# Kernel tuning notes

Hardware: AMD Instinct MI355X
Metric: run time of the kernel (lower is better)

## Reference

```python
import jax, jax.numpy as jnp
import numpy as np

LN_EPS = 1e-5  # torch LayerNorm default

def _phi(x):
    # elu(x) + 1 feature map
    return jax.nn.elu(x) + 1.0

def setup_inputs() -> dict:
    key = jax.random.key(0)
    ks = jax.random.split(key, 5)
    B, N, D = 4, 8192, 1024
    s = 1.0 / np.sqrt(D)
    return {
        "H": jax.random.normal(ks[0], (B, N, D), dtype=jnp.float32),
        "W_qkv": jax.random.normal(ks[1], (3 * D, D), dtype=jnp.float32) * s,
        "b_qkv": jax.random.normal(ks[2], (3 * D,), dtype=jnp.float32) * 0.01,
        "W_proj": jax.random.normal(ks[3], (D, D), dtype=jnp.float32) * s,
        "b_proj": jax.random.normal(ks[4], (D,), dtype=jnp.float32) * 0.01,
        "gamma": jnp.ones((D,), dtype=jnp.float32),
        "beta": jnp.zeros((D,), dtype=jnp.float32),
    }

def reference(H, W_qkv, b_qkv, W_proj, b_proj, gamma, beta):
    B, N, D = H.shape
    num_heads = 16
    head_dim = D // num_heads
    residual = H
    # qkv projection: (B,N,3D)
    qkv = jnp.einsum('bnd,ed->bne', H, W_qkv) + b_qkv
    qkv = qkv.reshape(B, N, 3, num_heads, head_dim).transpose(2, 0, 3, 1, 4)
    q, k, v = qkv[0], qkv[1], qkv[2]  # each (B,h,N,d)
    q = _phi(q)
    k = _phi(k)
    # kv outer-product accumulated over nodes: (B,h,d,v)
    kv = jnp.einsum('bhnd,bhnv->bhdv', k, v)
    k1 = k.sum(axis=2)  # (B,h,d)
    qkv_out = jnp.einsum('bhnd,bhdv->bhnv', q, kv)
    qk1 = jnp.sum(q * k1[:, :, None, :], axis=-1, keepdims=True)
    out = qkv_out / jnp.clip(qk1, 1e-6, None)
    # NOTE: faithful to original -- reshape (B,h,N,d) -> (B,N,D) WITHOUT head transpose
    out = out.reshape(B, N, D)
    out = jnp.einsum('bnd,ed->bne', out, W_proj) + b_proj
    # LayerNorm over last dim
    mu = out.mean(axis=-1, keepdims=True)
    var = out.var(axis=-1, keepdims=True)
    out = (out - mu) * jax.lax.rsqrt(var + LN_EPS) * gamma + beta
    # dropout is identity at inference
    return out + residual
```

## Files before the change

### kernel.cpp

```cpp
#include <hip/hip_runtime.h>


typedef __attribute__((ext_vector_type(4))) float f32x4;
typedef __attribute__((ext_vector_type(8))) short bf16x8;

__device__ __forceinline__ unsigned short f2b(float f) {
    unsigned u = __float_as_uint(f);
    u = (u + 0x7FFFu + ((u >> 16) & 1u)) >> 16;
    return (unsigned short)u;
}
__device__ __forceinline__ float b2f(unsigned short h) {
    return __uint_as_float(((unsigned)h) << 16);
}

__device__ __forceinline__ void glds16(const void* gp, void* lp) {
    __builtin_amdgcn_global_load_lds(
        (__attribute__((address_space(1))) void*)(unsigned long long)gp,
        (__attribute__((address_space(3))) void*)(unsigned int)(unsigned long long)lp,
        16, 0, 0);
}

__global__ __launch_bounds__(256) void cvt_f32_bf16(const float* __restrict__ in,
                                                    unsigned short* __restrict__ out,
                                                    long n4) {
    long i = (long)blockIdx.x * 256 + threadIdx.x;
    long stride = (long)gridDim.x * 256;
    for (; i < n4; i += stride) {
        float4 v = ((const float4*)in)[i];
        ushort4 o;
        o.x = f2b(v.x); o.y = f2b(v.y); o.z = f2b(v.z); o.w = f2b(v.w);
        ((ushort4*)out)[i] = o;
    }
}

template<int MODE>
__global__ __launch_bounds__(512) void gemm256(const unsigned short* __restrict__ A,
                                               const unsigned short* __restrict__ B,
                                               const float* __restrict__ bias,
                                               void* __restrict__ Cout,
                                               int mb, int N, int K) {
    __shared__ unsigned short lds[2][2][256][64];
    const int tid = threadIdx.x;
    const int wid = tid >> 6, lane = tid & 63;
    const int wr = wid >> 2, wc = wid & 3;
    const int lr = lane & 15, lq = lane >> 4;
    const int cpx = (int)gridDim.x >> 3;
    const int L = ((int)blockIdx.x & 7) * cpx + ((int)blockIdx.x >> 3);
    const int bm = L % mb, bn = L / mb;
    const size_t aRow0 = (size_t)bm * 256, bRow0 = (size_t)bn * 256;

    const int sr8 = lane >> 3;
    const int ssw = ((lane & 7) ^ sr8) * 8;
    const unsigned short* aG = A + (aRow0 + (size_t)(wid * 8 + sr8)) * K + ssw;
    const unsigned short* bG = B + (bRow0 + (size_t)(wid * 8 + sr8)) * K + ssw;

    f32x4 acc[8][4] = {};
    const char* base = (const char*)&lds[0][0][0][0];

    auto stage = [&](int buf, int k0) {
#pragma unroll
        for (int j = 0; j < 8; ++j) {
            const unsigned short* g = (j < 4 ? aG : bG) + (size_t)(j & 3) * 64 * K + k0;
            glds16(g, &lds[buf][j >> 2][(j & 3) * 64 + wid * 8][0]);
        }
    };
    auto ldA = [&](int cur, int mi, int ks) {
        int row = wr * 128 + mi * 16 + lr;
        int off = (cur * 2 + 0) * 32768 + row * 128 + ((((ks << 2) | lq) ^ (row & 7)) << 4);
        return *(const bf16x8*)(base + off);
    };
    auto ldB = [&](int cur, int ni, int ks) {
        int row = wc * 64 + ni * 16 + lr;
        int off = (cur * 2 + 1) * 32768 + row * 128 + ((((ks << 2) | lq) ^ (row & 7)) << 4);
        return *(const bf16x8*)(base + off);
    };

    const int nt = K >> 6;
    stage(0, 0);
    asm volatile("s_waitcnt vmcnt(0)" ::: "memory");
    __builtin_amdgcn_s_barrier();

    bf16x8 af[4][2], bfr[4][2];
    for (int t = 0; t < nt; ++t) {
        const int cur = t & 1;
#pragma unroll
        for (int mi = 0; mi < 4; ++mi) {
            af[mi][0] = ldA(cur, mi, 0); af[mi][1] = ldA(cur, mi, 1);
        }
#pragma unroll
        for (int ni = 0; ni < 2; ++ni) {
            bfr[ni][0] = ldB(cur, ni, 0); bfr[ni][1] = ldB(cur, ni, 1);
        }
        if (t + 1 < nt) stage(cur ^ 1, (t + 1) << 6);
        __builtin_amdgcn_s_barrier();
        __builtin_amdgcn_s_setprio(1);
#pragma unroll
        for (int mi = 0; mi < 4; ++mi)
#pragma unroll
            for (int ni = 0; ni < 2; ++ni)
#pragma unroll
                for (int ks = 0; ks < 2; ++ks)
                    acc[mi][ni] = __builtin_amdgcn_mfma_f32_16x16x32_bf16(
                        af[mi][ks], bfr[ni][ks], acc[mi][ni], 0, 0, 0);
        __builtin_amdgcn_s_setprio(0);
        __builtin_amdgcn_s_barrier();
#pragma unroll
        for (int ni = 2; ni < 4; ++ni) {
            bfr[ni][0] = ldB(cur, ni, 0); bfr[ni][1] = ldB(cur, ni, 1);
        }
        __builtin_amdgcn_s_barrier();
        __builtin_amdgcn_s_setprio(1);
#pragma unroll
        for (int mi = 0; mi < 4; ++mi)
#pragma unroll
            for (int ni = 2; ni < 4; ++ni)
#pragma unroll
                for (int ks = 0; ks < 2; ++ks)
                    acc[mi][ni] = __builtin_amdgcn_mfma_f32_16x16x32_bf16(
                        af[mi][ks], bfr[ni][ks], acc[mi][ni], 0, 0, 0);
        __builtin_amdgcn_s_setprio(0);
        __builtin_amdgcn_s_barrier();
#pragma unroll
        for (int mi = 0; mi < 4; ++mi) {
            af[mi][0] = ldA(cur, mi + 4, 0); af[mi][1] = ldA(cur, mi + 4, 1);
        }
        __builtin_amdgcn_s_barrier();
        __builtin_amdgcn_s_setprio(1);
#pragma unroll
        for (int mi = 0; mi < 4; ++mi)
#pragma unroll
            for (int ni = 2; ni < 4; ++ni)
#pragma unroll
                for (int ks = 0; ks < 2; ++ks)
                    acc[mi + 4][ni] = __builtin_amdgcn_mfma_f32_16x16x32_bf16(
                        af[mi][ks], bfr[ni][ks], acc[mi + 4][ni], 0, 0, 0);
        __builtin_amdgcn_s_setprio(0);
        __builtin_amdgcn_s_barrier();
        __builtin_amdgcn_s_setprio(1);
#pragma unroll
        for (int mi = 0; mi < 4; ++mi)
#pragma unroll
            for (int ni = 0; ni < 2; ++ni)
#pragma unroll
                for (int ks = 0; ks < 2; ++ks)
                    acc[mi + 4][ni] = __builtin_amdgcn_mfma_f32_16x16x32_bf16(
                        af[mi][ks], bfr[ni][ks], acc[mi + 4][ni], 0, 0, 0);
        __builtin_amdgcn_s_setprio(0);
        asm volatile("s_waitcnt vmcnt(0)" ::: "memory");
        __builtin_amdgcn_s_barrier();
        __builtin_amdgcn_sched_barrier(0);
    }
#pragma unroll
    for (int mi = 0; mi < 8; ++mi) {
#pragma unroll
        for (int ni = 0; ni < 4; ++ni) {
            int col = (int)bRow0 + wc * 64 + ni * 16 + lr;
            float bv = bias[col];
#pragma unroll
            for (int r = 0; r < 4; ++r) {
                size_t row = aRow0 + wr * 128 + mi * 16 + lq * 4 + r;
                float v = acc[mi][ni][r] + bv;
                if (MODE == 0) {
                    if (col < 2048) v = (v > 0.f) ? (v + 1.f) : __expf(v);
                    ((unsigned short*)Cout)[row * (size_t)N + col] = f2b(v);
                } else {
                    ((float*)Cout)[row * (size_t)N + col] = v;
                }
            }
        }
    }
}

__global__ __launch_bounds__(256) void kv_partial(const unsigned short* __restrict__ qkv,
                                                  float* __restrict__ part) {
    const int bh = blockIdx.x, chunk = blockIdx.y;
    const int b = bh >> 4, h = bh & 15;
    __shared__ unsigned short kb[16][64];
    __shared__ unsigned short vb[16][64];
    const int tid = threadIdx.x;
    const int d0 = (tid >> 4) * 4, v0 = (tid & 15) * 4;
    float acc[4][4] = {};
    float k1a[4] = {0.f, 0.f, 0.f, 0.f};
    const size_t base = ((size_t)b * 8192 + (size_t)chunk * 1024) * 3072;
    const int nn = tid >> 4;
    const int which = (tid >> 3) & 1;
    const int cg = tid & 7;
    const size_t loff = base + (size_t)nn * 3072 + (which ? 2048 : 1024) + h * 64 + cg * 8;

    for (int n0 = 0; n0 < 1024; n0 += 16) {
        uint4 val = *(const uint4*)(qkv + loff + (size_t)n0 * 3072);
        if (which) *(uint4*)(&vb[nn][cg * 8]) = val;
        else       *(uint4*)(&kb[nn][cg * 8]) = val;
        __syncthreads();
#pragma unroll 4
        for (int j = 0; j < 16; ++j) {
            ushort4 ku = *(const ushort4*)(&kb[j][d0]);
            ushort4 vu = *(const ushort4*)(&vb[j][v0]);
            float kd[4] = {b2f(ku.x), b2f(ku.y), b2f(ku.z), b2f(ku.w)};
            float vd[4] = {b2f(vu.x), b2f(vu.y), b2f(vu.z), b2f(vu.w)};
#pragma unroll
            for (int i = 0; i < 4; ++i)
#pragma unroll
                for (int jj = 0; jj < 4; ++jj)
                    acc[i][jj] += kd[i] * vd[jj];
            if ((tid & 15) == 0)
#pragma unroll
                for (int i = 0; i < 4; ++i) k1a[i] += kd[i];
        }
        __syncthreads();
    }
    float* dst = part + ((size_t)bh * 8 + chunk) * 4160;
#pragma unroll
    for (int i = 0; i < 4; ++i)
#pragma unroll
        for (int jj = 0; jj < 4; ++jj)
            dst[(d0 + i) * 64 + v0 + jj] = acc[i][jj];
    if ((tid & 15) == 0)
#pragma unroll
        for (int i = 0; i < 4; ++i) dst[4096 + d0 + i] = k1a[i];
}

__global__ __launch_bounds__(256) void kv_reduce(const float* __restrict__ part,
                                                 float* __restrict__ kvk1) {
    const int bh = blockIdx.x;
    for (int idx = threadIdx.x; idx < 4160; idx += 256) {
        float s = 0.f;
#pragma unroll
        for (int c = 0; c < 8; ++c) s += part[((size_t)bh * 8 + c) * 4160 + idx];
        kvk1[(size_t)bh * 4160 + idx] = s;
    }
}

__global__ __launch_bounds__(256) void apply_attn(const unsigned short* __restrict__ qkv,
                                                  const float* __restrict__ kvk1,
                                                  unsigned short* __restrict__ att) {
    const int nblk = blockIdx.x;
    const int bh = blockIdx.y;
    const int b = bh >> 4, h = bh & 15;
    __shared__ float kvs[64][64];
    __shared__ float k1s[64];
    const float* src = kvk1 + (size_t)bh * 4160;
    for (int i = threadIdx.x; i < 4096; i += 256) kvs[i >> 6][i & 63] = src[i];
    if (threadIdx.x < 64) k1s[threadIdx.x] = src[4096 + threadIdx.x];
    __syncthreads();
    const int t = threadIdx.x;
    const int r = t >> 2, qt = t & 3;
    const int n = nblk * 64 + r;
    const unsigned short* qrow = qkv + ((size_t)b * 8192 + n) * 3072 + h * 64;
    float acc[16] = {};
    float qk1 = 0.f;
    for (int dc = 0; dc < 64; dc += 8) {
        uint4 qu = *(const uint4*)(qrow + dc);
        unsigned qw[4] = {qu.x, qu.y, qu.z, qu.w};
#pragma unroll
        for (int jj = 0; jj < 8; ++jj) {
            float qd = (jj & 1) ? __uint_as_float(qw[jj >> 1] & 0xFFFF0000u)
                                : __uint_as_float(qw[jj >> 1] << 16);
            int d = dc + jj;
            qk1 += qd * k1s[d];
            const float4* kr = (const float4*)(&kvs[d][qt * 16]);
            float4 c0 = kr[0], c1 = kr[1], c2 = kr[2], c3 = kr[3];
            acc[0]  += qd * c0.x; acc[1]  += qd * c0.y; acc[2]  += qd * c0.z; acc[3]  += qd * c0.w;
            acc[4]  += qd * c1.x; acc[5]  += qd * c1.y; acc[6]  += qd * c1.z; acc[7]  += qd * c1.w;
            acc[8]  += qd * c2.x; acc[9]  += qd * c2.y; acc[10] += qd * c2.z; acc[11] += qd * c2.w;
            acc[12] += qd * c3.x; acc[13] += qd * c3.y; acc[14] += qd * c3.z; acc[15] += qd * c3.w;
        }
    }
    float rinv = 1.f / fmaxf(qk1, 1e-6f);
    union { unsigned short us[16]; uint4 u4[2]; } ob;
#pragma unroll
    for (int j = 0; j < 16; ++j) ob.us[j] = f2b(acc[j] * rinv);
    unsigned short* dst = att + (((size_t)b * 8192) + h * 512 + (n >> 4)) * 1024
                              + (n & 15) * 64 + qt * 16;
    *(uint4*)dst = ob.u4[0];
    *(uint4*)(dst + 8) = ob.u4[1];
}

__global__ __launch_bounds__(256) void ln_residual(const float* __restrict__ X,
                                                   const float* __restrict__ H,
                                                   const float* __restrict__ gamma,
                                                   const float* __restrict__ beta,
                                                   float* __restrict__ out) {
    const size_t row = blockIdx.x;
    const int tid = threadIdx.x;
    const float* x = X + row * 1024;
    float v[4];
    float s = 0.f, s2 = 0.f;
#pragma unroll
    for (int i = 0; i < 4; ++i) {
        v[i] = x[tid + i * 256];
        s += v[i];
        s2 += v[i] * v[i];
    }
#pragma unroll
    for (int o = 32; o > 0; o >>= 1) {
        s  += __shfl_xor(s, o, 64);
        s2 += __shfl_xor(s2, o, 64);
    }
    __shared__ float rs[4], rs2[4];
    const int wave = tid >> 6;
    if ((tid & 63) == 0) { rs[wave] = s; rs2[wave] = s2; }
    __syncthreads();
    s  = rs[0] + rs[1] + rs[2] + rs[3];
    s2 = rs2[0] + rs2[1] + rs2[2] + rs2[3];
    float mu = s * (1.f / 1024.f);
    float var = s2 * (1.f / 1024.f) - mu * mu;
    float inv = rsqrtf(var + 1e-5f);
    const float* hrow = H + row * 1024;
    float* orow = out + row * 1024;
#pragma unroll
    for (int i = 0; i < 4; ++i) {
        int c = tid + i * 256;
        orow[c] = (v[i] - mu) * inv * gamma[c] + beta[c] + hrow[c];
    }
}

extern "C" void kernel_launch(void* const* d_in, const int* in_sizes, int n_in,
                              void* d_out, int out_size, void* d_ws, size_t ws_size,
                              hipStream_t stream) {
    const float* H     = (const float*)d_in[0];
    const float* Wqkv  = (const float*)d_in[1];
    const float* bqkv  = (const float*)d_in[2];
    const float* Wproj = (const float*)d_in[3];
    const float* bproj = (const float*)d_in[4];
    const float* gamma = (const float*)d_in[5];
    const float* beta  = (const float*)d_in[6];
    float* out = (float*)d_out;
    char* ws = (char*)d_ws;

    unsigned short* wq_bf = (unsigned short*)(ws);
    unsigned short* wp_bf = (unsigned short*)(ws + 6291456);
    unsigned short* hbf   = (unsigned short*)(ws + 8388608);
    unsigned short* att   = hbf;
    unsigned short* qkvbf = (unsigned short*)(ws + 75497472);
    float*          out2  = (float*)(ws + 75497472);
    float*          kvk1  = (float*)(ws + 276824064);
    float*          part  = (float*)(ws + 277889024);

    cvt_f32_bf16<<<2048, 256, 0, stream>>>(H, hbf, 33554432 / 4);
    cvt_f32_bf16<<<256, 256, 0, stream>>>(Wqkv, wq_bf, 3145728 / 4);
    cvt_f32_bf16<<<128, 256, 0, stream>>>(Wproj, wp_bf, 1048576 / 4);

    gemm256<0><<<1536, 512, 0, stream>>>(hbf, wq_bf, bqkv, (void*)qkvbf,
                                         128, 3072, 1024);

    kv_partial<<<dim3(64, 8), 256, 0, stream>>>(qkvbf, part);
    kv_reduce<<<64, 256, 0, stream>>>(part, kvk1);

    apply_attn<<<dim3(128, 64), 256, 0, stream>>>(qkvbf, kvk1, att);

    gemm256<1><<<512, 512, 0, stream>>>(att, wp_bf, bproj, (void*)out2,
                                        128, 1024, 1024);

    ln_residual<<<32768, 256, 0, stream>>>(out2, H, gamma, beta, out);
}
```

Before: 635.9 us.

## Store projection output as bf16, merge conversions, and use wave-per-row LayerNorm

The output projection GEMM now writes bf16 instead of fp32, which halves its store traffic and the LayerNorm read traffic. The LayerNorm kernel now gives one wave per row in a grid-stride loop and uses vectorized float4 and ushort4 accesses, with no block-level shared-memory reduction. The three fp32-to-bf16 conversion launches are merged into one kernel that splits its blocks across the three tensors. Rounding the pre-LayerNorm activations to bf16 costs some precision.

```diff
diff --git a/kernel.cpp b/kernel.cpp
--- a/kernel.cpp
+++ b/kernel.cpp
@@ -20,16 +20,24 @@
         16, 0, 0);
 }
 
-__global__ __launch_bounds__(256) void cvt_f32_bf16(const float* __restrict__ in,
-                                                    unsigned short* __restrict__ out,
-                                                    long n4) {
-    long i = (long)blockIdx.x * 256 + threadIdx.x;
-    long stride = (long)gridDim.x * 256;
+__global__ __launch_bounds__(256) void cvt_all(const float* __restrict__ H,
+                                               const float* __restrict__ Wq,
+                                               const float* __restrict__ Wp,
+                                               unsigned short* __restrict__ hbf,
+                                               unsigned short* __restrict__ wqb,
+                                               unsigned short* __restrict__ wpb) {
+    const int blk = blockIdx.x;
+    const float* src; unsigned short* dst; long n4; int b0, nb;
+    if (blk < 1792)      { src = H;  dst = hbf; n4 = 8388608; b0 = 0;    nb = 1792; }
+    else if (blk < 1920) { src = Wq; dst = wqb; n4 = 786432;  b0 = 1792; nb = 128; }
+    else                 { src = Wp; dst = wpb; n4 = 262144;  b0 = 1920; nb = 64; }
+    long i = (long)(blk - b0) * 256 + threadIdx.x;
+    const long stride = (long)nb * 256;
     for (; i < n4; i += stride) {
-        float4 v = ((const float4*)in)[i];
+        float4 v = ((const float4*)src)[i];
         ushort4 o;
         o.x = f2b(v.x); o.y = f2b(v.y); o.z = f2b(v.z); o.w = f2b(v.w);
-        ((ushort4*)out)[i] = o;
+        ((ushort4*)dst)[i] = o;
     }
 }
 
@@ -162,10 +170,8 @@
                 float v = acc[mi][ni][r] + bv;
                 if (MODE == 0) {
                     if (col < 2048) v = (v > 0.f) ? (v + 1.f) : __expf(v);
-                    ((unsigned short*)Cout)[row * (size_t)N + col] = f2b(v);
-                } else {
-                    ((float*)Cout)[row * (size_t)N + col] = v;
                 }
+                ((unsigned short*)Cout)[row * (size_t)N + col] = f2b(v);
             }
         }
     }
@@ -276,42 +282,50 @@
     *(uint4*)(dst + 8) = ob.u4[1];
 }
 
-__global__ __launch_bounds__(256) void ln_residual(const float* __restrict__ X,
+__global__ __launch_bounds__(256) void ln_residual(const unsigned short* __restrict__ X,
                                                    const float* __restrict__ H,
                                                    const float* __restrict__ gamma,
                                                    const float* __restrict__ beta,
-                                                   float* __restrict__ out) {
-    const size_t row = blockIdx.x;
-    const int tid = threadIdx.x;
-    const float* x = X + row * 1024;
-    float v[4];
-    float s = 0.f, s2 = 0.f;
-#pragma unroll
-    for (int i = 0; i < 4; ++i) {
-        v[i] = x[tid + i * 256];
-        s += v[i];
-        s2 += v[i] * v[i];
-    }
-#pragma unroll
-    for (int o = 32; o > 0; o >>= 1) {
-        s  += __shfl_xor(s, o, 64);
-        s2 += __shfl_xor(s2, o, 64);
-    }
-    __shared__ float rs[4], rs2[4];
-    const int wave = tid >> 6;
-    if ((tid & 63) == 0) { rs[wave] = s; rs2[wave] = s2; }
-    __syncthreads();
-    s  = rs[0] + rs[1] + rs[2] + rs[3];
-    s2 = rs2[0] + rs2[1] + rs2[2] + rs2[3];
-    float mu = s * (1.f / 1024.f);
-    float var = s2 * (1.f / 1024.f) - mu * mu;
-    float inv = rsqrtf(var + 1e-5f);
-    const float* hrow = H + row * 1024;
-    float* orow = out + row * 1024;
-#pragma unroll
-    for (int i = 0; i < 4; ++i) {
-        int c = tid + i * 256;
-        orow[c] = (v[i] - mu) * inv * gamma[c] + beta[c] + hrow[c];
+                                                   float* __restrict__ out,
+                                                   int nrows) {
+    const int lane = threadIdx.x & 63;
+    int row = blockIdx.x * 4 + (threadIdx.x >> 6);
+    const int rstride = gridDim.x * 4;
+    for (; row < nrows; row += rstride) {
+        const unsigned short* x = X + (size_t)row * 1024;
+        float v[16];
+        float s = 0.f, s2 = 0.f;
+#pragma unroll
+        for (int j = 0; j < 4; ++j) {
+            ushort4 u = *(const ushort4*)(x + j * 256 + lane * 4);
+            float a = b2f(u.x), b = b2f(u.y), c = b2f(u.z), d = b2f(u.w);
+            v[j * 4 + 0] = a; v[j * 4 + 1] = b; v[j * 4 + 2] = c; v[j * 4 + 3] = d;
+            s += a + b + c + d;
+            s2 += a * a + b * b + c * c + d * d;
+        }
+#pragma unroll
+        for (int o = 32; o > 0; o >>= 1) {
+            s  += __shfl_xor(s, o, 64);
+            s2 += __shfl_xor(s2, o, 64);
+        }
+        const float mu = s * (1.f / 1024.f);
+        const float var = s2 * (1.f / 1024.f) - mu * mu;
+        const float inv = rsqrtf(var + 1e-5f);
+        const float* hrow = H + (size_t)row * 1024;
+        float* orow = out + (size_t)row * 1024;
+#pragma unroll
+        for (int j = 0; j < 4; ++j) {
+            const int c = j * 256 + lane * 4;
+            float4 g = *(const float4*)(gamma + c);
+            float4 bt = *(const float4*)(beta + c);
+            float4 hr = *(const float4*)(hrow + c);
+            float4 o;
+            o.x = (v[j * 4 + 0] - mu) * inv * g.x + bt.x + hr.x;
+            o.y = (v[j * 4 + 1] - mu) * inv * g.y + bt.y + hr.y;
+            o.z = (v[j * 4 + 2] - mu) * inv * g.z + bt.z + hr.z;
+            o.w = (v[j * 4 + 3] - mu) * inv * g.w + bt.w + hr.w;
+            *(float4*)(orow + c) = o;
+        }
     }
 }
 
@@ -333,13 +347,11 @@
     unsigned short* hbf   = (unsigned short*)(ws + 8388608);
     unsigned short* att   = hbf;
     unsigned short* qkvbf = (unsigned short*)(ws + 75497472);
-    float*          out2  = (float*)(ws + 75497472);
+    unsigned short* out2  = (unsigned short*)(ws + 75497472);
     float*          kvk1  = (float*)(ws + 276824064);
     float*          part  = (float*)(ws + 277889024);
 
-    cvt_f32_bf16<<<2048, 256, 0, stream>>>(H, hbf, 33554432 / 4);
-    cvt_f32_bf16<<<256, 256, 0, stream>>>(Wqkv, wq_bf, 3145728 / 4);
-    cvt_f32_bf16<<<128, 256, 0, stream>>>(Wproj, wp_bf, 1048576 / 4);
+    cvt_all<<<1984, 256, 0, stream>>>(H, Wqkv, Wproj, hbf, wq_bf, wp_bf);
 
     gemm256<0><<<1536, 512, 0, stream>>>(hbf, wq_bf, bqkv, (void*)qkvbf,
                                          128, 3072, 1024);
@@ -352,5 +364,5 @@
     gemm256<1><<<512, 512, 0, stream>>>(att, wp_bf, bproj, (void*)out2,
                                         128, 1024, 1024);
 
-    ln_residual<<<32768, 256, 0, stream>>>(out2, H, gamma, beta, out);
-}
+    ln_residual<<<2048, 256, 0, stream>>>(out2, H, gamma, beta, out, 32768);
+}
```

Result: faster. 605.4 us (-4.8%).
